# Kernel optimization log

Measured on AMD Instinct MI355X. Metric: run time of the kernel, lower is better.

The kernel has to match this reference:

```python
import jax, jax.numpy as jnp
import numpy as np

B, S, D, H = 4, 2048, 768, 4
DH = D // H  # 192


def setup_inputs() -> dict:
    key = jax.random.key(0)
    ks = jax.random.split(key, 5)
    std = 1.0 / np.sqrt(D)
    return {
        "x": jax.random.normal(ks[0], (B, S, D), dtype=jnp.float32),
        "Wq": jax.random.normal(ks[1], (D, D), dtype=jnp.float32) * std,
        "Wk": jax.random.normal(ks[2], (D, D), dtype=jnp.float32) * std,
        "Wv": jax.random.normal(ks[3], (D, D), dtype=jnp.float32) * std,
        "Wo": jax.random.normal(ks[4], (D, D), dtype=jnp.float32) * std,
    }


def reference(x, Wq, Wk, Wv, Wo):
    b, s, d = x.shape
    # nn.Linear(bias=False): y = x @ W.T
    q = (x @ Wq.T).reshape(b, s, H, DH).transpose(0, 2, 1, 3)  # [B,H,S,DH]
    k = (x @ Wk.T).reshape(b, s, H, DH).transpose(0, 2, 1, 3)
    v = (x @ Wv.T).reshape(b, s, H, DH).transpose(0, 2, 1, 3)
    scale = jnp.sqrt(jnp.asarray(DH, dtype=q.dtype))
    logits = jnp.einsum("bhqd,bhkd->bhqk", q, k) / scale  # [B,H,S,S]
    causal = jnp.tril(jnp.ones((s, s), dtype=bool))
    logits = jnp.where(causal, logits, -jnp.inf)
    A = jax.nn.softmax(logits, axis=-1)
    preout = jnp.einsum("bhqk,bhkd->bhqd", A, v)  # [B,H,S,DH]
    # W_O = rearrange(Wo.T, '(h dh) dm -> h dh dm'); sum over heads == full Wo
    W_O = Wo.T.reshape(H, DH, D)
    out = jnp.einsum("bhsd,hdm->bsm", preout, W_O)  # [B,S,D]
    return out
```

## Files before the change

kernel.cpp:

```cpp
#include <hip/hip_runtime.h>
#include <hip/hip_bf16.h>

constexpr int CB = 4, CS = 2048, CD = 768, CH = 4, CDH = 192;
constexpr int CM = CB * CS;

typedef float f32x4 __attribute__((ext_vector_type(4)));
typedef float fx4 __attribute__((ext_vector_type(4)));
typedef __bf16 bx8 __attribute__((ext_vector_type(8)));
typedef unsigned short u16;
typedef u16 u16x8 __attribute__((ext_vector_type(8)));
typedef u16 u16x4 __attribute__((ext_vector_type(4)));

static __device__ __forceinline__ u16 f32_bf16(float f) {
  unsigned u = __builtin_bit_cast(unsigned, f);
  u += 0x7FFFu + ((u >> 16) & 1u);
  return (u16)(u >> 16);
}

static __device__ __forceinline__ f32x4 mfma16(bx8 a, bx8 b, f32x4 c) {
  return __builtin_amdgcn_mfma_f32_16x16x32_bf16(a, b, c, 0, 0, 0);
}

__global__ void __launch_bounds__(256) convert_all(
    const float* __restrict__ x, const float* __restrict__ wq,
    const float* __restrict__ wk, const float* __restrict__ wv,
    const float* __restrict__ wo, u16* __restrict__ xb, u16* __restrict__ wqb,
    u16* __restrict__ wkb, u16* __restrict__ wvb, u16* __restrict__ wob) {
  const float* srcs[5] = {x, wq, wk, wv, wo};
  u16* dsts[5] = {xb, wqb, wkb, wvb, wob};
  const int n4s[5] = {CM * CD / 4, CD * CD / 4, CD * CD / 4, CD * CD / 4,
                      CD * CD / 4};
  const int gsz = gridDim.x * blockDim.x;
  const int gid = blockIdx.x * blockDim.x + threadIdx.x;
#pragma unroll
  for (int sg = 0; sg < 5; ++sg) {
    const fx4* src = (const fx4*)srcs[sg];
    u16* dst = dsts[sg];
    const int n4 = n4s[sg];
    for (int i = gid; i < n4; i += gsz) {
      fx4 v = src[i];
      u16x4 o;
      o[0] = f32_bf16(v[0]);
      o[1] = f32_bf16(v[1]);
      o[2] = f32_bf16(v[2]);
      o[3] = f32_bf16(v[3]);
      *(u16x4*)&dst[(size_t)i * 4] = o;
    }
  }
}

template <bool OUT_BF16>
__global__ void __launch_bounds__(256) gemm_bt(
    const u16* __restrict__ A, const u16* __restrict__ Bw0,
    const u16* __restrict__ Bw1, const u16* __restrict__ Bw2,
    void* __restrict__ C0, void* __restrict__ C1, void* __restrict__ C2,
    int M, int N, int K) {
  constexpr int LDK = 72;
  __shared__ u16 As[128][LDK];
  __shared__ u16 Bs[128][LDK];
  const int z = blockIdx.z;
  const u16* Bw = (z == 0) ? Bw0 : ((z == 1) ? Bw1 : Bw2);
  void* Cv = (z == 0) ? C0 : ((z == 1) ? C1 : C2);
  const int m0 = blockIdx.x * 128;
  const int n0 = blockIdx.y * 128;
  const int tid = threadIdx.x;
  const int wave = tid >> 6, lane = tid & 63;
  const int wr = wave >> 1, wc = wave & 1;
  const int lr = lane & 15, lhi = lane >> 4;

  f32x4 acc[4][4];
  const f32x4 zero = {0.f, 0.f, 0.f, 0.f};
#pragma unroll
  for (int i = 0; i < 4; ++i)
#pragma unroll
    for (int j = 0; j < 4; ++j) acc[i][j] = zero;

  for (int kk = 0; kk < K; kk += 64) {
#pragma unroll
    for (int r = 0; r < 4; ++r) {
      const int id = tid + r * 256;
      const int row = id >> 3, ch = id & 7;
      *(u16x8*)&As[row][ch * 8] =
          *(const u16x8*)&A[(size_t)(m0 + row) * K + kk + ch * 8];
      *(u16x8*)&Bs[row][ch * 8] =
          *(const u16x8*)&Bw[(size_t)(n0 + row) * K + kk + ch * 8];
    }
    __syncthreads();
#pragma unroll
    for (int ks = 0; ks < 2; ++ks) {
      bx8 af[4], bf[4];
#pragma unroll
      for (int mf = 0; mf < 4; ++mf)
        af[mf] = *(const bx8*)&As[wr * 64 + mf * 16 + lr][ks * 32 + lhi * 8];
#pragma unroll
      for (int nf = 0; nf < 4; ++nf)
        bf[nf] = *(const bx8*)&Bs[wc * 64 + nf * 16 + lr][ks * 32 + lhi * 8];
#pragma unroll
      for (int mf = 0; mf < 4; ++mf)
#pragma unroll
        for (int nf = 0; nf < 4; ++nf)
          acc[mf][nf] = mfma16(af[mf], bf[nf], acc[mf][nf]);
    }
    __syncthreads();
  }
#pragma unroll
  for (int mf = 0; mf < 4; ++mf)
#pragma unroll
    for (int nf = 0; nf < 4; ++nf)
#pragma unroll
      for (int r = 0; r < 4; ++r) {
        const int row = m0 + wr * 64 + mf * 16 + lhi * 4 + r;
        const int col = n0 + wc * 64 + nf * 16 + lr;
        if constexpr (OUT_BF16)
          ((u16*)Cv)[(size_t)row * N + col] = f32_bf16(acc[mf][nf][r]);
        else
          ((float*)Cv)[(size_t)row * N + col] = acc[mf][nf][r];
      }
}

__global__ void __launch_bounds__(256, 2) flash_attn(
    const u16* __restrict__ Qg, const u16* __restrict__ Kg,
    const u16* __restrict__ Vg, u16* __restrict__ Og) {
  __shared__ u16 Ks[12288];
  __shared__ u16 Vs[12288];
  __shared__ u16 Ps[4][16][72];
  const int g = blockIdx.x;
  const int qt = (g < 256) ? (g >> 4) : (31 - ((g - 256) >> 4));
  const int bh = g & 15;
  const int b = bh >> 2, h = bh & 3;
  const int tid = threadIdx.x;
  const int wave = tid >> 6, lane = tid & 63;
  const int lr = lane & 15, lhi = lane >> 4;
  const size_t base_elem = ((size_t)b * CS) * CD + (size_t)h * CDH;
  constexpr float scale = 0.07216878364870323f;
  const f32x4 zero = {0.f, 0.f, 0.f, 0.f};

  int kOff[6], vOff[6];
#pragma unroll
  for (int r = 0; r < 6; ++r) {
    const int p = tid + r * 256;
    {
      const int k = p / 24, c16 = p - k * 24;
      const unsigned swz = ((unsigned)(c16 * 16)) ^ ((unsigned)((k & 7) << 4));
      kOff[r] = k * CD + (int)(swz >> 1);
    }
    {
      const int blk = p >> 3, kq = (p >> 1) & 3, dh = p & 1;
      const int kk = ((blk & 15) << 2) + kq;
      const int d = ((blk >> 4) << 4) + dh * 8;
      vOff[r] = kk * CD + d;
    }
  }
  const unsigned vlds0 =
      (unsigned)(unsigned long long)(__attribute__((address_space(3)))
                                         u16*)&Vs[0];

  float m_run = -INFINITY, l_run = 0.f;
  f32x4 acc[12];
#pragma unroll
  for (int nf = 0; nf < 12; ++nf) acc[nf] = zero;

  bx8 qf[6];
  {
    const size_t qoff = base_elem + (size_t)(qt * 64 + wave * 16 + lr) * CD;
#pragma unroll
    for (int c = 0; c < 6; ++c)
      qf[c] = *(const bx8*)&Qg[qoff + c * 32 + lhi * 8];
  }

  u16x8 kreg[6], vreg[6];
  auto ldregs = [&](int kt) {
    const u16* kg = Kg + base_elem + (size_t)(kt * 64) * CD;
    const u16* vg = Vg + base_elem + (size_t)(kt * 64) * CD;
#pragma unroll
    for (int r = 0; r < 6; ++r) {
      kreg[r] = *(const u16x8*)&kg[kOff[r]];
      vreg[r] = *(const u16x8*)&vg[vOff[r]];
    }
  };

  ldregs(0);
  const int qg = qt * 64 + wave * 16 + lr;

  for (int i = 0; i <= qt; ++i) {
    __syncthreads();
#pragma unroll
    for (int r = 0; r < 6; ++r) {
      *(u16x8*)&Ks[(size_t)(tid + r * 256) * 8] = kreg[r];
      *(u16x8*)&Vs[(size_t)(tid + r * 256) * 8] = vreg[r];
    }
    if (i < qt) ldregs(i + 1);
    __syncthreads();

    const int k0 = i * 64;
    const bool diag = (i == qt);
    f32x4 st[4];
#pragma unroll
    for (int mf = 0; mf < 4; ++mf) st[mf] = zero;
#pragma unroll
    for (int c = 0; c < 6; ++c)
#pragma unroll
      for (int mf = 0; mf < 4; ++mf) {
        const int row = mf * 16 + lr;
        const unsigned off =
            ((unsigned)(c * 64 + lhi * 16)) ^ ((unsigned)((row & 7) << 4));
        const bx8 kf =
            *(const bx8*)((const char*)Ks + (size_t)row * 384 + off);
        st[mf] = mfma16(kf, qf[c], st[mf]);
      }
    float pvv[16];
#pragma unroll
    for (int mf = 0; mf < 4; ++mf)
#pragma unroll
      for (int r = 0; r < 4; ++r) {
        float s = st[mf][r] * scale;
        if (diag && (k0 + mf * 16 + lhi * 4 + r > qg)) s = -INFINITY;
        pvv[mf * 4 + r] = s;
      }
    float mx = pvv[0];
#pragma unroll
    for (int t = 1; t < 16; ++t) mx = fmaxf(mx, pvv[t]);
    mx = fmaxf(mx, __shfl_xor(mx, 16, 64));
    mx = fmaxf(mx, __shfl_xor(mx, 32, 64));
    const bool skip = __all(mx - m_run <= 8.0f);
    if (!skip) {
      const float mnew = fmaxf(m_run, mx);
      const float alpha = __expf(m_run - mnew);
      float afr[4];
#pragma unroll
      for (int r = 0; r < 4; ++r) afr[r] = __shfl(alpha, lhi * 4 + r, 64);
#pragma unroll
      for (int nf = 0; nf < 12; ++nf)
#pragma unroll
        for (int r = 0; r < 4; ++r) acc[nf][r] *= afr[r];
      l_run *= alpha;
      m_run = mnew;
    }
    float rs = 0.f;
#pragma unroll
    for (int t = 0; t < 16; ++t) {
      const float e = __expf(pvv[t] - m_run);
      pvv[t] = e;
      rs += e;
    }
    rs += __shfl_xor(rs, 16, 64);
    rs += __shfl_xor(rs, 32, 64);
    l_run += rs;
#pragma unroll
    for (int mf = 0; mf < 4; ++mf)
#pragma unroll
      for (int rp = 0; rp < 2; ++rp) {
        const unsigned w0 = f32_bf16(pvv[mf * 4 + rp * 2]);
        const unsigned w1 = f32_bf16(pvv[mf * 4 + rp * 2 + 1]);
        *(unsigned*)&Ps[wave][lr][mf * 16 + lhi * 4 + rp * 2] =
            w0 | (w1 << 16);
      }
    const bx8 pf0 = *(const bx8*)&Ps[wave][lr][lhi * 8];
    const bx8 pf1 = *(const bx8*)&Ps[wave][lr][32 + lhi * 8];
#pragma unroll
    for (int gg = 0; gg < 3; ++gg) {
      u16x4 tl[4][2], th[4][2];
#pragma unroll
      for (int q4 = 0; q4 < 4; ++q4)
#pragma unroll
        for (int c2 = 0; c2 < 2; ++c2) {
          const int nf = gg * 4 + q4;
          const unsigned va =
              vlds0 + (unsigned)((nf * 16 + c2 * 8 + lhi * 2) * 128 + lr * 8);
          asm volatile("ds_read_b64_tr_b16 %0, %2\n\t"
                       "ds_read_b64_tr_b16 %1, %2 offset:128"
                       : "=&v"(tl[q4][c2]), "=&v"(th[q4][c2])
                       : "v"(va));
        }
      asm volatile("s_waitcnt lgkmcnt(0)" ::: "memory");
      __builtin_amdgcn_sched_barrier(0);
#pragma unroll
      for (int q4 = 0; q4 < 4; ++q4)
#pragma unroll
        for (int c2 = 0; c2 < 2; ++c2) {
          const int nf = gg * 4 + q4;
          const u16x8 vv = __builtin_shufflevector(tl[q4][c2], th[q4][c2], 0,
                                                   1, 2, 3, 4, 5, 6, 7);
          acc[nf] = mfma16(c2 == 0 ? pf0 : pf1, __builtin_bit_cast(bx8, vv),
                           acc[nf]);
        }
    }
  }

#pragma unroll
  for (int r = 0; r < 4; ++r) {
    const float lb = __shfl(l_run, lhi * 4 + r, 64);
    const float linv = 1.0f / lb;
    const size_t orow =
        base_elem + (size_t)(qt * 64 + wave * 16 + lhi * 4 + r) * CD;
#pragma unroll
    for (int nf = 0; nf < 12; ++nf)
      Og[orow + nf * 16 + lr] = f32_bf16(acc[nf][r] * linv);
  }
}

extern "C" void kernel_launch(void* const* d_in, const int* in_sizes, int n_in,
                              void* d_out, int out_size, void* d_ws,
                              size_t ws_size, hipStream_t stream) {
  (void)in_sizes;
  (void)n_in;
  (void)out_size;
  (void)ws_size;
  const float* x = (const float*)d_in[0];
  const float* wq = (const float*)d_in[1];
  const float* wk = (const float*)d_in[2];
  const float* wv = (const float*)d_in[3];
  const float* wo = (const float*)d_in[4];
  float* out = (float*)d_out;
  char* ws = (char*)d_ws;
  const size_t big = (size_t)CM * CD * 2;
  const size_t wsz = (size_t)CD * CD * 2;
  u16* xb = (u16*)ws;
  u16* qb = (u16*)(ws + big);
  u16* kb = (u16*)(ws + 2 * big);
  u16* vb = (u16*)(ws + 3 * big);
  u16* wqb = (u16*)(ws + 4 * big);
  u16* wkb = (u16*)(ws + 4 * big + wsz);
  u16* wvb = (u16*)(ws + 4 * big + 2 * wsz);
  u16* wob = (u16*)(ws + 4 * big + 3 * wsz);
  u16* pob = xb;

  convert_all<<<dim3(1024), dim3(256), 0, stream>>>(x, wq, wk, wv, wo, xb, wqb,
                                                    wkb, wvb, wob);
  gemm_bt<true><<<dim3(64, 6, 3), dim3(256), 0, stream>>>(
      xb, wqb, wkb, wvb, (void*)qb, (void*)kb, (void*)vb, CM, CD, CD);
  flash_attn<<<dim3(512), dim3(256), 0, stream>>>(qb, kb, vb, pob);
  gemm_bt<false><<<dim3(64, 6, 1), dim3(256), 0, stream>>>(
      pob, wob, wob, wob, (void*)out, (void*)out, (void*)out, CM, CD, CD);
}
```

Before: 158.9 us.

## Fuse fp32-to-bf16 conversion into GEMM loads and split-KV balance flash attention

Removes the standalone conversion kernel: the GEMMs now read fp32 x and weights and convert to bf16 while staging tiles into shared memory. Flash attention is restructured so each block pair shares the work of a low and a high query tile, splitting the long high tiles' KV range across two blocks. The partial outputs and max/sum values are merged in a new combine kernel, using the output buffer as scratch. It also adds s_setprio around the MFMA sections. The aim is better load balance across the causal triangle and one fewer launch, at the cost of extra partial-output traffic, a combine pass, and redundant weight conversion in every GEMM block.

```diff
diff --git a/kernel.cpp b/kernel.cpp
--- a/kernel.cpp
+++ b/kernel.cpp
@@ -16,50 +16,37 @@
   u += 0x7FFFu + ((u >> 16) & 1u);
   return (u16)(u >> 16);
 }
+static __device__ __forceinline__ float bf16_f32(u16 v) {
+  return __builtin_bit_cast(float, (unsigned)v << 16);
+}
+static __device__ __forceinline__ u16x8 cvt8(fx4 a, fx4 b) {
+  u16x8 o;
+  o[0] = f32_bf16(a[0]);
+  o[1] = f32_bf16(a[1]);
+  o[2] = f32_bf16(a[2]);
+  o[3] = f32_bf16(a[3]);
+  o[4] = f32_bf16(b[0]);
+  o[5] = f32_bf16(b[1]);
+  o[6] = f32_bf16(b[2]);
+  o[7] = f32_bf16(b[3]);
+  return o;
+}
 
 static __device__ __forceinline__ f32x4 mfma16(bx8 a, bx8 b, f32x4 c) {
   return __builtin_amdgcn_mfma_f32_16x16x32_bf16(a, b, c, 0, 0, 0);
 }
 
-__global__ void __launch_bounds__(256) convert_all(
-    const float* __restrict__ x, const float* __restrict__ wq,
-    const float* __restrict__ wk, const float* __restrict__ wv,
-    const float* __restrict__ wo, u16* __restrict__ xb, u16* __restrict__ wqb,
-    u16* __restrict__ wkb, u16* __restrict__ wvb, u16* __restrict__ wob) {
-  const float* srcs[5] = {x, wq, wk, wv, wo};
-  u16* dsts[5] = {xb, wqb, wkb, wvb, wob};
-  const int n4s[5] = {CM * CD / 4, CD * CD / 4, CD * CD / 4, CD * CD / 4,
-                      CD * CD / 4};
-  const int gsz = gridDim.x * blockDim.x;
-  const int gid = blockIdx.x * blockDim.x + threadIdx.x;
-#pragma unroll
-  for (int sg = 0; sg < 5; ++sg) {
-    const fx4* src = (const fx4*)srcs[sg];
-    u16* dst = dsts[sg];
-    const int n4 = n4s[sg];
-    for (int i = gid; i < n4; i += gsz) {
-      fx4 v = src[i];
-      u16x4 o;
-      o[0] = f32_bf16(v[0]);
-      o[1] = f32_bf16(v[1]);
-      o[2] = f32_bf16(v[2]);
-      o[3] = f32_bf16(v[3]);
-      *(u16x4*)&dst[(size_t)i * 4] = o;
-    }
-  }
-}
-
-template <bool OUT_BF16>
+template <bool A_F32, bool OUT_BF16>
 __global__ void __launch_bounds__(256) gemm_bt(
-    const u16* __restrict__ A, const u16* __restrict__ Bw0,
-    const u16* __restrict__ Bw1, const u16* __restrict__ Bw2,
+    const void* __restrict__ A, const float* __restrict__ Bw0,
+    const float* __restrict__ Bw1, const float* __restrict__ Bw2,
     void* __restrict__ C0, void* __restrict__ C1, void* __restrict__ C2,
     int M, int N, int K) {
   constexpr int LDK = 72;
   __shared__ u16 As[128][LDK];
   __shared__ u16 Bs[128][LDK];
   const int z = blockIdx.z;
-  const u16* Bw = (z == 0) ? Bw0 : ((z == 1) ? Bw1 : Bw2);
+  const float* Bw = (z == 0) ? Bw0 : ((z == 1) ? Bw1 : Bw2);
   void* Cv = (z == 0) ? C0 : ((z == 1) ? C1 : C2);
   const int m0 = blockIdx.x * 128;
   const int n0 = blockIdx.y * 128;
@@ -80,10 +67,17 @@
     for (int r = 0; r < 4; ++r) {
       const int id = tid + r * 256;
       const int row = id >> 3, ch = id & 7;
-      *(u16x8*)&As[row][ch * 8] =
-          *(const u16x8*)&A[(size_t)(m0 + row) * K + kk + ch * 8];
-      *(u16x8*)&Bs[row][ch * 8] =
-          *(const u16x8*)&Bw[(size_t)(n0 + row) * K + kk + ch * 8];
+      u16x8 av;
+      if constexpr (A_F32) {
+        const float* ap = (const float*)A + (size_t)(m0 + row) * K + kk + ch * 8;
+        av = cvt8(*(const fx4*)ap, *(const fx4*)(ap + 4));
+      } else {
+        av = *(const u16x8*)((const u16*)A + (size_t)(m0 + row) * K + kk +
+                             ch * 8);
+      }
+      *(u16x8*)&As[row][ch * 8] = av;
+      const float* bp = Bw + (size_t)(n0 + row) * K + kk + ch * 8;
+      *(u16x8*)&Bs[row][ch * 8] = cvt8(*(const fx4*)bp, *(const fx4*)(bp + 4));
     }
     __syncthreads();
 #pragma unroll
@@ -120,13 +114,18 @@
 
 __global__ void __launch_bounds__(256, 2) flash_attn(
     const u16* __restrict__ Qg, const u16* __restrict__ Kg,
-    const u16* __restrict__ Vg, u16* __restrict__ Og) {
+    const u16* __restrict__ Vg, u16* __restrict__ Og, u16* __restrict__ paO,
+    float* __restrict__ paML, u16* __restrict__ pbO,
+    float* __restrict__ pbML) {
   __shared__ u16 Ks[12288];
   __shared__ u16 Vs[12288];
   __shared__ u16 Ps[4][16][72];
   const int g = blockIdx.x;
-  const int qt = (g < 256) ? (g >> 4) : (31 - ((g - 256) >> 4));
-  const int bh = g & 15;
+  const int bh = g >> 5;
+  const int t = (g >> 1) & 15;
+  const int roleB = g & 1;
+  const int qtLo = t, qtHi = 31 - t;
+  const int slot = bh * 16 + (15 - t);
   const int b = bh >> 2, h = bh & 3;
   const int tid = threadIdx.x;
   const int wave = tid >> 6, lane = tid & 63;
@@ -155,20 +154,18 @@
       (unsigned)(unsigned long long)(__attribute__((address_space(3)))
                                          u16*)&Vs[0];
 
-  float m_run = -INFINITY, l_run = 0.f;
+  float m_run, l_run;
   f32x4 acc[12];
-#pragma unroll
-  for (int nf = 0; nf < 12; ++nf) acc[nf] = zero;
-
   bx8 qf[6];
-  {
+  u16x8 kreg[6], vreg[6];
+
+  auto qload = [&](int qt) {
     const size_t qoff = base_elem + (size_t)(qt * 64 + wave * 16 + lr) * CD;
 #pragma unroll
     for (int c = 0; c < 6; ++c)
       qf[c] = *(const bx8*)&Qg[qoff + c * 32 + lhi * 8];
-  }
-
-  u16x8 kreg[6], vreg[6];
+  };
+
   auto ldregs = [&](int kt) {
     const u16* kg = Kg + base_elem + (size_t)(kt * 64) * CD;
     const u16* vg = Vg + base_elem + (size_t)(kt * 64) * CD;
@@ -179,24 +176,14 @@
     }
   };
 
-  ldregs(0);
-  const int qg = qt * 64 + wave * 16 + lr;
-
-  for (int i = 0; i <= qt; ++i) {
-    __syncthreads();
-#pragma unroll
-    for (int r = 0; r < 6; ++r) {
-      *(u16x8*)&Ks[(size_t)(tid + r * 256) * 8] = kreg[r];
-      *(u16x8*)&Vs[(size_t)(tid + r * 256) * 8] = vreg[r];
-    }
-    if (i < qt) ldregs(i + 1);
-    __syncthreads();
-
+  auto compute = [&](int i, int qt) {
+    const int qg = qt * 64 + wave * 16 + lr;
     const int k0 = i * 64;
     const bool diag = (i == qt);
     f32x4 st[4];
 #pragma unroll
     for (int mf = 0; mf < 4; ++mf) st[mf] = zero;
+    __builtin_amdgcn_s_setprio(1);
 #pragma unroll
     for (int c = 0; c < 6; ++c)
 #pragma unroll
@@ -208,6 +195,7 @@
             *(const bx8*)((const char*)Ks + (size_t)row * 384 + off);
         st[mf] = mfma16(kf, qf[c], st[mf]);
       }
+    __builtin_amdgcn_s_setprio(0);
     float pvv[16];
 #pragma unroll
     for (int mf = 0; mf < 4; ++mf)
@@ -219,7 +207,7 @@
       }
     float mx = pvv[0];
 #pragma unroll
-    for (int t = 1; t < 16; ++t) mx = fmaxf(mx, pvv[t]);
+    for (int tt = 1; tt < 16; ++tt) mx = fmaxf(mx, pvv[tt]);
     mx = fmaxf(mx, __shfl_xor(mx, 16, 64));
     mx = fmaxf(mx, __shfl_xor(mx, 32, 64));
     const bool skip = __all(mx - m_run <= 8.0f);
@@ -238,9 +226,9 @@
     }
     float rs = 0.f;
 #pragma unroll
-    for (int t = 0; t < 16; ++t) {
-      const float e = __expf(pvv[t] - m_run);
-      pvv[t] = e;
+    for (int tt = 0; tt < 16; ++tt) {
+      const float e = __expf(pvv[tt] - m_run);
+      pvv[tt] = e;
       rs += e;
     }
     rs += __shfl_xor(rs, 16, 64);
@@ -274,6 +262,7 @@
         }
       asm volatile("s_waitcnt lgkmcnt(0)" ::: "memory");
       __builtin_amdgcn_sched_barrier(0);
+      __builtin_amdgcn_s_setprio(1);
 #pragma unroll
       for (int q4 = 0; q4 < 4; ++q4)
 #pragma unroll
@@ -284,18 +273,113 @@
           acc[nf] = mfma16(c2 == 0 ? pf0 : pf1, __builtin_bit_cast(bx8, vv),
                            acc[nf]);
         }
+      __builtin_amdgcn_s_setprio(0);
+    }
+  };
+
+  auto run = [&](int qt, int i0, int i1) {
+    m_run = -INFINITY;
+    l_run = 0.f;
+#pragma unroll
+    for (int nf = 0; nf < 12; ++nf) acc[nf] = zero;
+    qload(qt);
+    ldregs(i0);
+    for (int i = i0; i <= i1; ++i) {
+      __syncthreads();
+#pragma unroll
+      for (int r = 0; r < 6; ++r) {
+        *(u16x8*)&Ks[(size_t)(tid + r * 256) * 8] = kreg[r];
+        *(u16x8*)&Vs[(size_t)(tid + r * 256) * 8] = vreg[r];
+      }
+      if (i < i1) ldregs(i + 1);
+      __syncthreads();
+      compute(i, qt);
+    }
+  };
+
+  auto final_epilogue = [&](int qt) {
+#pragma unroll
+    for (int r = 0; r < 4; ++r) {
+      const float lb = __shfl(l_run, lhi * 4 + r, 64);
+      const float linv = 1.0f / lb;
+      const size_t orow =
+          base_elem + (size_t)(qt * 64 + wave * 16 + lhi * 4 + r) * CD;
+#pragma unroll
+      for (int nf = 0; nf < 12; ++nf)
+        Og[orow + nf * 16 + lr] = f32_bf16(acc[nf][r] * linv);
+    }
+  };
+
+  auto partial_epilogue = [&](u16* pO, float* pML) {
+    if (lhi == 0) {
+      pML[slot * 128 + wave * 16 + lr] = m_run;
+      pML[slot * 128 + 64 + wave * 16 + lr] = l_run;
+    }
+#pragma unroll
+    for (int r = 0; r < 4; ++r) {
+      const float lb = __shfl(l_run, lhi * 4 + r, 64);
+      const float linv = 1.0f / lb;
+      u16* dst =
+          pO + (size_t)slot * 12288 + (size_t)(wave * 16 + lhi * 4 + r) * 192;
+#pragma unroll
+      for (int nf = 0; nf < 12; ++nf)
+        dst[nf * 16 + lr] = f32_bf16(acc[nf][r] * linv);
+    }
+  };
+
+  if (roleB) {
+    run(qtHi, 15 - t, 31 - t);
+    partial_epilogue(pbO, pbML);
+  } else {
+    run(qtLo, 0, t);
+    final_epilogue(qtLo);
+    if (t < 15) {
+      run(qtHi, 0, 14 - t);
+      partial_epilogue(paO, paML);
+    } else {
+      if (tid < 64) {
+        paML[slot * 128 + tid] = -1e30f;
+        paML[slot * 128 + 64 + tid] = 0.f;
+      }
     }
   }
-
-#pragma unroll
-  for (int r = 0; r < 4; ++r) {
-    const float lb = __shfl(l_run, lhi * 4 + r, 64);
-    const float linv = 1.0f / lb;
-    const size_t orow =
-        base_elem + (size_t)(qt * 64 + wave * 16 + lhi * 4 + r) * CD;
-#pragma unroll
-    for (int nf = 0; nf < 12; ++nf)
-      Og[orow + nf * 16 + lr] = f32_bf16(acc[nf][r] * linv);
+}
+
+__global__ void __launch_bounds__(256) combine_qt(
+    const u16* __restrict__ paO, const float* __restrict__ paML,
+    const u16* __restrict__ pbO, const float* __restrict__ pbML,
+    u16* __restrict__ Og) {
+  const int s = blockIdx.x;
+  const int bh = s >> 4;
+  const int qtHi = 16 + (s & 15);
+  const int b = bh >> 2, h = bh & 3;
+  const int tid = threadIdx.x;
+  const int row = tid >> 2, cg = tid & 3;
+  const float mA = paML[s * 128 + row], lA = paML[s * 128 + 64 + row];
+  const float mB = pbML[s * 128 + row], lB = pbML[s * 128 + 64 + row];
+  const size_t obase =
+      ((size_t)b * CS + (size_t)qtHi * 64 + row) * CD + h * CDH + cg * 48;
+  const u16* pa = paO + (size_t)s * 12288 + (size_t)row * 192 + cg * 48;
+  const u16* pb = pbO + (size_t)s * 12288 + (size_t)row * 192 + cg * 48;
+  if (lA > 0.f) {
+    const float M = fmaxf(mA, mB);
+    const float wA = lA * __expf(mA - M), wB = lB * __expf(mB - M);
+    const float inv = 1.0f / (wA + wB);
+    const float fa = wA * inv, fb = wB * inv;
+#pragma unroll
+    for (int c = 0; c < 6; ++c) {
+      const u16x8 va = *(const u16x8*)&pa[c * 8];
+      const u16x8 vb = *(const u16x8*)&pb[c * 8];
+      u16x8 o;
+#pragma unroll
+      for (int j = 0; j < 8; ++j)
+        o[j] = f32_bf16(fa * bf16_f32(va[j]) + fb * bf16_f32(vb[j]));
+      *(u16x8*)&Og[obase + c * 8] = o;
+    }
+  } else {
+#pragma unroll
+    for (int c = 0; c < 6; ++c)
+      *(u16x8*)&Og[obase + c * 8] = *(const u16x8*)&pb[c * 8];
   }
 }
 
@@ -314,22 +398,22 @@
   float* out = (float*)d_out;
   char* ws = (char*)d_ws;
   const size_t big = (size_t)CM * CD * 2;
-  const size_t wsz = (size_t)CD * CD * 2;
-  u16* xb = (u16*)ws;
+  u16* pob = (u16*)ws;
   u16* qb = (u16*)(ws + big);
   u16* kb = (u16*)(ws + 2 * big);
   u16* vb = (u16*)(ws + 3 * big);
-  u16* wqb = (u16*)(ws + 4 * big);
-  u16* wkb = (u16*)(ws + 4 * big + wsz);
-  u16* wvb = (u16*)(ws + 4 * big + 2 * wsz);
-  u16* wob = (u16*)(ws + 4 * big + 3 * wsz);
-  u16* pob = xb;
-
-  convert_all<<<dim3(1024), dim3(256), 0, stream>>>(x, wq, wk, wv, wo, xb, wqb,
-                                                    wkb, wvb, wob);
-  gemm_bt<true><<<dim3(64, 6, 3), dim3(256), 0, stream>>>(
-      xb, wqb, wkb, wvb, (void*)qb, (void*)kb, (void*)vb, CM, CD, CD);
-  flash_attn<<<dim3(512), dim3(256), 0, stream>>>(qb, kb, vb, pob);
-  gemm_bt<false><<<dim3(64, 6, 1), dim3(256), 0, stream>>>(
-      pob, wob, wob, wob, (void*)out, (void*)out, (void*)out, CM, CD, CD);
-}
+  const size_t pOsz = (size_t)256 * 64 * 192 * 2;
+  u16* paO = (u16*)d_out;
+  u16* pbO = (u16*)((char*)d_out + pOsz);
+  float* paML = (float*)((char*)d_out + 2 * pOsz);
+  float* pbML = (float*)((char*)d_out + 2 * pOsz + 131072);
+
+  gemm_bt<true, true><<<dim3(64, 6, 3), dim3(256), 0, stream>>>(
+      (const void*)x, wq, wk, wv, (void*)qb, (void*)kb, (void*)vb, CM, CD, CD);
+  flash_attn<<<dim3(512), dim3(256), 0, stream>>>(qb, kb, vb, pob, paO, paML,
+                                                  pbO, pbML);
+  combine_qt<<<dim3(256), dim3(256), 0, stream>>>(paO, paML, pbO, pbML, pob);
+  gemm_bt<false, false><<<dim3(64, 6, 1), dim3(256), 0, stream>>>(
+      (const void*)pob, wo, wo, wo, (void*)out, (void*)out, (void*)out, CM, CD,
+      CD);
+}
```

New measurement: 196.1 us. +23.4%, slower.
